# Kernel optimization log

Measured on AMD Instinct MI355X. Metric: run time of the kernel, lower is better.

## Reference

```python
import jax, jax.numpy as jnp
import numpy as np

B, LQ, S, D, H = 8, 1024, 256, 1024, 16
HD = D // H
LN_EPS = 1e-5


def layer_norm(x, g, b):
    m = jnp.mean(x, axis=-1, keepdims=True)
    v = jnp.mean((x - m) ** 2, axis=-1, keepdims=True)
    return (x - m) / jnp.sqrt(v + LN_EPS) * g + b


def setup_inputs() -> dict:
    key = jax.random.key(0)
    ks = jax.random.split(key, 12)
    sc = 0.02
    p = lambda k, shp: jax.random.normal(k, shp, dtype=jnp.float32) * sc
    return {
        "memory": jax.random.normal(ks[0], (B, LQ, D // 2), dtype=jnp.float32),
        "gaze_features": jax.random.normal(ks[1], (B, LQ, D // 2), dtype=jnp.float32),
        "text_features": jax.random.normal(ks[2], (B, S, D), dtype=jnp.float32),
        "w_in": p(ks[3], (3 * D, D)),  # packed q,k,v in_proj (torch MHA layout)
        "b_in": jnp.zeros((3 * D,), jnp.float32),
        "w_o": p(ks[4], (D, D)),
        "b_o": jnp.zeros((D,), jnp.float32),
        "w1": p(ks[5], (D, D)),
        "b1": jnp.zeros((D,), jnp.float32),
        "w2": p(ks[6], (D, D)),
        "b2": jnp.zeros((D,), jnp.float32),
        "g1": jnp.ones((D,), jnp.float32),
        "be1": jnp.zeros((D,), jnp.float32),
        "g2": jnp.ones((D,), jnp.float32),
        "be2": jnp.zeros((D,), jnp.float32),
    }


def reference(memory, gaze_features, text_features, w_in, b_in, w_o, b_o,
              w1, b1, w2, b2, g1, be1, g2, be2):
    combined = jnp.concatenate([memory, gaze_features], axis=-1)  # [B, LQ, D]
    wq, wk, wv = w_in[:D], w_in[D:2 * D], w_in[2 * D:]
    bq, bk, bv = b_in[:D], b_in[D:2 * D], b_in[2 * D:]

    q = (combined @ wq.T + bq).reshape(B, LQ, H, HD)
    k = (text_features @ wk.T + bk).reshape(B, S, H, HD)
    v = (text_features @ wv.T + bv).reshape(B, S, H, HD)

    scores = jnp.einsum("bqhd,bkhd->bhqk", q, k) / jnp.sqrt(jnp.float32(HD))
    attn_w = jax.nn.softmax(scores, axis=-1)
    ctx = jnp.einsum("bhqk,bkhd->bqhd", attn_w, v).reshape(B, LQ, D)
    attn_output = ctx @ w_o.T + b_o  # [B, LQ, D]

    # dual FFN branches share linear1/linear2 (as in the source); dropout = eval identity
    ffn = jax.nn.relu(attn_output @ w1.T + b1) @ w2.T + b2
    refpoint_embed = layer_norm(ffn, g1, be1)
    tgt = layer_norm(ffn, g2, be2)

    # vectorized box decode (replaces the per-element Python loop)
    s = jax.nn.sigmoid(attn_output[..., :4])
    xc, yc, w, h = s[..., 0], s[..., 1], s[..., 2], s[..., 3]
    init_box_proposal = jnp.stack(
        [xc - w / 2, yc - h / 2, xc + w / 2, yc + h / 2], axis=-1)  # [B, LQ, 4]

    return refpoint_embed, tgt, init_box_proposal
```

## Files before the change

kernel.cpp:

```cpp
#include <hip/hip_runtime.h>


typedef unsigned short u16;
typedef unsigned int u32;
typedef __bf16 bf16x8 __attribute__((ext_vector_type(8)));
typedef float f32x4 __attribute__((ext_vector_type(4)));
typedef u16 u16x4 __attribute__((ext_vector_type(4)));

struct CvtArgs { const void* in[15]; };

__device__ __forceinline__ u16 f2bf(float f) {
  u32 u = __builtin_bit_cast(u32, f);
  u += 0x7fffu + ((u >> 16) & 1u);
  return (u16)(u >> 16);
}
__device__ __forceinline__ float bf2f(u16 h) {
  u32 u = ((u32)h) << 16;
  return __builtin_bit_cast(float, u);
}

struct WsPtrs {
  u16 *c_mem, *c_gaze, *c_text, *c_win, *c_bin, *c_wo, *c_bo, *c_w1, *c_b1,
      *c_w2, *c_b2, *c_g1, *c_be1, *c_g2, *c_be2;
  u16 *q, *k, *v, *ctx, *woT, *wf, *bfb, *h1, *ffnb;
};
__device__ __forceinline__ WsPtrs wsp(u16* C) {
  WsPtrs w;
  w.c_mem = C;                 w.c_gaze = C + 4194304;   w.c_text = C + 8388608;
  w.c_win = C + 10485760;      w.c_bin = C + 13631488;   w.c_wo = C + 13634560;
  w.c_bo = C + 14683136;       w.c_w1 = C + 14684160;    w.c_b1 = C + 15732736;
  w.c_w2 = C + 15733760;       w.c_b2 = C + 16782336;    w.c_g1 = C + 16783360;
  w.c_be1 = C + 16784384;      w.c_g2 = C + 16785408;    w.c_be2 = C + 16786432;
  u16* B2 = C + 16787488;
  w.q = B2;                    w.k = B2 + 8388608;       w.v = B2 + 10485760;
  w.ctx = B2 + 12582912;
  w.woT = B2 + 20971520;
  w.wf  = B2 + 22020096;
  w.bfb = B2 + 23068672;
  w.h1  = B2 + 29360128;
  w.ffnb = B2;
  return w;
}

__device__ __forceinline__ void cvt_chunk(bool f32in, u16* dst,
                                          const void* const* srcs, u32 c8) {
  const u32 cum[16] = {0u, 4194304u, 8388608u, 10485760u, 13631488u, 13634560u,
                       14683136u, 14684160u, 15732736u, 15733760u, 16782336u,
                       16783360u, 16784384u, 16785408u, 16786432u, 16787456u};
  u32 base = c8 * 8u;
  int idx = 0;
#pragma unroll
  for (int i = 1; i < 15; ++i) if (base >= cum[i]) idx = i;
  u32 off = base - cum[idx];
  if (f32in) {
    const float* s = (const float*)srcs[idx] + off;
    float4 a = ((const float4*)s)[0];
    float4 b = ((const float4*)s)[1];
    u16 t[8] = {f2bf(a.x), f2bf(a.y), f2bf(a.z), f2bf(a.w),
                f2bf(b.x), f2bf(b.y), f2bf(b.z), f2bf(b.w)};
    *(uint4*)(dst + base) = *(const uint4*)t;
  } else {
    *(uint4*)(dst + base) = *(const uint4*)((const u16*)srcs[idx] + off);
  }
}

__global__ __launch_bounds__(256) void cvt_tr(CvtArgs a, u16* ws) {
  __shared__ u16 tile[128 * 136];
  const bool f32in = (((const u32*)a.in[11])[0] == 0x3F800000u);
  const int bid = blockIdx.x, tid = threadIdx.x;
  if (bid < 64) {
    WsPtrs w = wsp(ws);
    int tr = bid >> 3, tc = bid & 7;
#pragma unroll
    for (int p = 0; p < 8; ++p) {
      int t = p * 16 + (tid >> 4);
      int j8 = (tid & 15) * 8;
      u16 tmp[8];
      if (f32in) {
        const float* s = (const float*)a.in[5] + (size_t)(tr * 128 + t) * 1024 + tc * 128 + j8;
        float4 x = ((const float4*)s)[0], y = ((const float4*)s)[1];
        tmp[0]=f2bf(x.x); tmp[1]=f2bf(x.y); tmp[2]=f2bf(x.z); tmp[3]=f2bf(x.w);
        tmp[4]=f2bf(y.x); tmp[5]=f2bf(y.y); tmp[6]=f2bf(y.z); tmp[7]=f2bf(y.w);
      } else {
        *(uint4*)tmp = *(const uint4*)((const u16*)a.in[5] + (size_t)(tr * 128 + t) * 1024 + tc * 128 + j8);
      }
      *(uint4*)&tile[t * 136 + j8] = *(const uint4*)tmp;
    }
    __syncthreads();
#pragma unroll
    for (int p = 0; p < 8; ++p) {
      int j = p * 16 + (tid >> 4);
      int t8 = (tid & 15) * 8;
      u16 tmp[8];
#pragma unroll
      for (int i = 0; i < 8; ++i) tmp[i] = tile[(t8 + i) * 136 + j];
      *(uint4*)(w.woT + (size_t)(tc * 128 + j) * 1024 + tr * 128 + t8) = *(const uint4*)tmp;
    }
  } else {
    u32 c8 = (u32)(bid - 64) * 256u + tid;
    if (c8 < 2098432u) cvt_chunk(f32in, ws, a.in, c8);
  }
}

__device__ __forceinline__ void gemm_core(
    u16* sA, u16* sB,
    const u16* A0, const u16* A1, int Ksplit, int lda0, int lda1,
    const u16* W, const u16* bias, void* out, int N, int K,
    int mode, int lg, int m0, int n0)
{
  const int tid = threadIdx.x;
  const int wave = tid >> 6, lane = tid & 63;
  const int quad = lane >> 4, l16 = lane & 15;
  const int wm = wave >> 1, wn = wave & 1;

  f32x4 acc[4][4];
#pragma unroll
  for (int i = 0; i < 4; ++i)
#pragma unroll
    for (int j = 0; j < 4; ++j) acc[i][j] = (f32x4){0.f, 0.f, 0.f, 0.f};

  for (int k0 = 0; k0 < K; k0 += 64) {
#pragma unroll
    for (int qi = 0; qi < 4; ++qi) {
      int p = (wave * 4 + qi) * 64 + lane;
      int row = p >> 3;
      int c = (p & 7) ^ (row & 7);
      int gk = k0 + (c << 3);
      const u16* srcA = (gk < Ksplit) ? (A0 + (size_t)(m0 + row) * lda0 + gk)
                                      : (A1 + (size_t)(m0 + row) * lda1 + (gk - Ksplit));
      __builtin_amdgcn_global_load_lds(
          (const __attribute__((address_space(1))) void*)srcA,
          (__attribute__((address_space(3))) void*)&sA[(size_t)(wave * 4 + qi) * 512],
          16, 0, 0);
      const u16* srcB = W + (size_t)(n0 + row) * K + gk;
      __builtin_amdgcn_global_load_lds(
          (const __attribute__((address_space(1))) void*)srcB,
          (__attribute__((address_space(3))) void*)&sB[(size_t)(wave * 4 + qi) * 512],
          16, 0, 0);
    }
    __syncthreads();
#pragma unroll
    for (int ks = 0; ks < 2; ++ks) {
      const int ch = (ks << 2) + quad;
      bf16x8 af[4], bw[4];
#pragma unroll
      for (int i = 0; i < 4; ++i) {
        int row = wm * 64 + i * 16 + l16;
        af[i] = *(const bf16x8*)&sA[(row << 6) + ((ch ^ (row & 7)) << 3)];
      }
#pragma unroll
      for (int j = 0; j < 4; ++j) {
        int row = wn * 64 + j * 16 + l16;
        bw[j] = *(const bf16x8*)&sB[(row << 6) + ((ch ^ (row & 7)) << 3)];
      }
#pragma unroll
      for (int i = 0; i < 4; ++i)
#pragma unroll
        for (int j = 0; j < 4; ++j)
          acc[i][j] = __builtin_amdgcn_mfma_f32_16x16x32_bf16(af[i], bw[j], acc[i][j], 0, 0, 0);
    }
    __syncthreads();
  }

#pragma unroll
  for (int i = 0; i < 4; ++i) {
#pragma unroll
    for (int j = 0; j < 4; ++j) {
      int n = n0 + wn * 64 + j * 16 + l16;
      float bv = bias ? bf2f(bias[n]) : 0.f;
#pragma unroll
      for (int rr = 0; rr < 4; ++rr) {
        int m = m0 + wm * 64 + i * 16 + quad * 4 + rr;
        float val = acc[i][j][rr] + bv;
        if (mode == 1) val = fmaxf(val, 0.f);
        if (mode <= 1) {
          ((u16*)out)[(size_t)m * N + n] = f2bf(val);
        } else if (mode == 3) {
          int b = m >> lg, l = m & ((1 << lg) - 1);
          int h = n >> 6, d = n & 63;
          ((u16*)out)[((size_t)((b * 16 + h)) << (lg + 6)) + (l << 6) + d] = f2bf(val);
        } else {
          int b = m >> lg, s = m & ((1 << lg) - 1);
          int h = n >> 6, d = n & 63;
          ((u16*)out)[((size_t)(((b * 16 + h) << 6) + d) << lg) + s] = f2bf(val);
        }
      }
    }
  }
}

__global__ __launch_bounds__(256, 4) void qkvwf(u16* ws) {
  __shared__ __align__(16) u16 lds[16384];
  WsPtrs w = wsp(ws);
  const int bid = blockIdx.x, tid = threadIdx.x;
  if (bid < 512) {
    gemm_core(lds, lds + 8192, w.c_mem, w.c_gaze, 512, 512, 512,
              w.c_win, w.c_bin, w.q, 1024, 1024, 3, 10,
              (bid >> 3) * 128, (bid & 7) * 128);
  } else if (bid < 640) {
    int u = bid - 512;
    gemm_core(lds, lds + 8192, w.c_text, w.c_text, 1024, 1024, 1024,
              w.c_win + 1048576, w.c_bin + 1024, w.k, 1024, 1024, 3, 8,
              (u >> 3) * 128, (u & 7) * 128);
  } else if (bid < 768) {
    int u = bid - 640;
    gemm_core(lds, lds + 8192, w.c_text, w.c_text, 1024, 1024, 1024,
              w.c_win + 2097152, w.c_bin + 2048, w.v, 1024, 1024, 4, 8,
              (u >> 3) * 128, (u & 7) * 128);
  } else if (bid < 832) {
    int u = bid - 768;
    gemm_core(lds, lds + 8192, w.c_w1, w.c_w1, 1024, 1024, 1024,
              w.woT, nullptr, w.wf, 1024, 1024, 0, 0,
              (u >> 3) * 128, (u & 7) * 128);
  } else {
    int i = (bid - 832) * 256 + tid;
    const u16* w1row = w.c_w1 + (size_t)i * 1024;
    float acc = bf2f(w.c_b1[i]);
    for (int kk = 0; kk < 1024; kk += 8) {
      bf16x8 wv = *(const bf16x8*)(w1row + kk);
      bf16x8 bv = *(const bf16x8*)(w.c_bo + kk);
#pragma unroll
      for (int j = 0; j < 8; ++j) acc += (float)wv[j] * (float)bv[j];
    }
    w.bfb[i] = f2bf(acc);
  }
}

__global__ __launch_bounds__(256) void attn_kernel(u16* ws) {
  __shared__ u16 sV[64 * 256];
  __shared__ u16 sKP[256 * 64];
  WsPtrs w = wsp(ws);
  const int tid = threadIdx.x;
  const int wave = tid >> 6, lane = tid & 63;
  const int quad = lane >> 4, l16 = lane & 15;
  const int qb = blockIdx.x & 15, bh = blockIdx.x >> 4;

  {
    int rr = tid >> 3, c8 = (tid & 7) << 3;
    const u16* kb = w.k + (size_t)bh * 16384;
#pragma unroll
    for (int p = 0; p < 8; ++p) {
      int row = p * 32 + rr;
      uint4 val = *(const uint4*)(kb + row * 64 + c8);
      *(uint4*)&sKP[(row << 6) + ((((c8 >> 3) ^ (row & 7))) << 3)] = val;
    }
    int r2 = tid >> 5, c8b = (tid & 31) << 3;
    const u16* vb = w.v + (size_t)bh * 16384;
#pragma unroll
    for (int p = 0; p < 8; ++p) {
      int row = p * 8 + r2;
      uint4 val = *(const uint4*)(vb + (row << 8) + c8b);
      *(uint4*)&sV[(row << 8) + ((((c8b >> 3) ^ (row & 7))) << 3)] = val;
    }
  }
  bf16x8 aq[2];
  {
    const u16* qrow = w.q + ((size_t)bh * 1024 + qb * 64 + wave * 16 + l16) * 64 + quad * 8;
    aq[0] = *(const bf16x8*)(qrow);
    aq[1] = *(const bf16x8*)(qrow + 32);
  }
  __syncthreads();

  f32x4 sc[16];
#pragma unroll
  for (int nt = 0; nt < 16; ++nt) sc[nt] = (f32x4){0.f, 0.f, 0.f, 0.f};
#pragma unroll
  for (int ks = 0; ks < 2; ++ks) {
    const int ch = (ks << 2) + quad;
#pragma unroll
    for (int nt = 0; nt < 16; ++nt) {
      int row = nt * 16 + l16;
      bf16x8 bk = *(const bf16x8*)&sKP[(row << 6) + ((ch ^ (row & 7)) << 3)];
      sc[nt] = __builtin_amdgcn_mfma_f32_16x16x32_bf16(aq[ks], bk, sc[nt], 0, 0, 0);
    }
  }
#pragma unroll
  for (int rr = 0; rr < 4; ++rr) {
    float mx = -1e30f;
#pragma unroll
    for (int nt = 0; nt < 16; ++nt) mx = fmaxf(mx, sc[nt][rr]);
    for (int off = 1; off < 16; off <<= 1) mx = fmaxf(mx, __shfl_xor(mx, off, 64));
    float sum = 0.f;
#pragma unroll
    for (int nt = 0; nt < 16; ++nt) {
      float p = __expf((sc[nt][rr] - mx) * 0.125f);
      sc[nt][rr] = p; sum += p;
    }
    for (int off = 1; off < 16; off <<= 1) sum += __shfl_xor(sum, off, 64);
    float inv = 1.f / sum;
#pragma unroll
    for (int nt = 0; nt < 16; ++nt) sc[nt][rr] *= inv;
  }
  __syncthreads();
#pragma unroll
  for (int nt = 0; nt < 16; ++nt)
#pragma unroll
    for (int rr = 0; rr < 4; ++rr) {
      int row = wave * 16 + quad * 4 + rr;
      int col = nt * 16 + l16;
      sKP[(row << 8) + (((col >> 3) ^ (row & 7)) << 3) + (col & 7)] = f2bf(sc[nt][rr]);
    }
  __syncthreads();

  f32x4 o[4];
#pragma unroll
  for (int j = 0; j < 4; ++j) o[j] = (f32x4){0.f, 0.f, 0.f, 0.f};
#pragma unroll
  for (int ks = 0; ks < 8; ++ks) {
    const int ch = (ks << 2) + quad;
    int prow = wave * 16 + l16;
    bf16x8 ap = *(const bf16x8*)&sKP[(prow << 8) + ((ch ^ (prow & 7)) << 3)];
#pragma unroll
    for (int j = 0; j < 4; ++j) {
      int vrow = j * 16 + l16;
      bf16x8 bv = *(const bf16x8*)&sV[(vrow << 8) + ((ch ^ (vrow & 7)) << 3)];
      o[j] = __builtin_amdgcn_mfma_f32_16x16x32_bf16(ap, bv, o[j], 0, 0, 0);
    }
  }
  const int b = bh >> 4, h = bh & 15;
#pragma unroll
  for (int j = 0; j < 4; ++j)
#pragma unroll
    for (int rr = 0; rr < 4; ++rr) {
      int m = qb * 64 + wave * 16 + quad * 4 + rr;
      int d = h * 64 + j * 16 + l16;
      w.ctx[((size_t)b * 1024 + m) * 1024 + d] = f2bf(o[j][rr]);
    }
}

__global__ __launch_bounds__(256, 4) void h1box(u16* ws, void* out, const void* g1orig) {
  __shared__ __align__(16) u16 lds[16384];
  WsPtrs w = wsp(ws);
  const int u = blockIdx.x, tid = threadIdx.x;
  const int r16 = tid >> 4, l4 = tid & 15;
  {
    const bool f32out = (((const u32*)g1orig)[0] == 0x3F800000u);
    int m = u * 16 + r16;
    int k0 = l4 * 64;
    const u16* crow = w.ctx + (size_t)m * 1024 + k0;
    float a0 = 0.f, a1 = 0.f, a2 = 0.f, a3 = 0.f;
#pragma unroll
    for (int kk = 0; kk < 64; kk += 8) {
      bf16x8 cv = *(const bf16x8*)(crow + kk);
      bf16x8 w0 = *(const bf16x8*)(w.c_wo + k0 + kk);
      bf16x8 w1 = *(const bf16x8*)(w.c_wo + 1024 + k0 + kk);
      bf16x8 w2 = *(const bf16x8*)(w.c_wo + 2048 + k0 + kk);
      bf16x8 w3 = *(const bf16x8*)(w.c_wo + 3072 + k0 + kk);
#pragma unroll
      for (int j = 0; j < 8; ++j) {
        float c = (float)cv[j];
        a0 += c * (float)w0[j]; a1 += c * (float)w1[j];
        a2 += c * (float)w2[j]; a3 += c * (float)w3[j];
      }
    }
    for (int off = 1; off < 16; off <<= 1) {
      a0 += __shfl_xor(a0, off, 64); a1 += __shfl_xor(a1, off, 64);
      a2 += __shfl_xor(a2, off, 64); a3 += __shfl_xor(a3, off, 64);
    }
    if (l4 == 0) {
      a0 += bf2f(w.c_bo[0]); a1 += bf2f(w.c_bo[1]);
      a2 += bf2f(w.c_bo[2]); a3 += bf2f(w.c_bo[3]);
      float s0 = 1.f / (1.f + __expf(-a0)), s1 = 1.f / (1.f + __expf(-a1));
      float s2 = 1.f / (1.f + __expf(-a2)), s3 = 1.f / (1.f + __expf(-a3));
      float o0 = s0 - s2 * 0.5f, o1 = s1 - s3 * 0.5f;
      float o2 = s0 + s2 * 0.5f, o3 = s1 + s3 * 0.5f;
      if (f32out) {
        float* fo = (float*)out + 16777216;
        *(float4*)(fo + (size_t)m * 4) = make_float4(o0, o1, o2, o3);
      } else {
        u16* bo = (u16*)out + 16777216;
        u16x4 o; o[0] = f2bf(o0); o[1] = f2bf(o1); o[2] = f2bf(o2); o[3] = f2bf(o3);
        *(u16x4*)(bo + (size_t)m * 4) = o;
      }
    }
  }
  gemm_core(lds, lds + 8192, w.ctx, w.ctx, 1024, 1024, 1024,
            w.wf, w.bfb, w.h1, 1024, 1024, 1, 0, (u >> 3) * 128, (u & 7) * 128);
}

__global__ __launch_bounds__(256, 4) void w2gemm(u16* ws) {
  __shared__ __align__(16) u16 lds[16384];
  WsPtrs w = wsp(ws);
  gemm_core(lds, lds + 8192, w.h1, w.h1, 1024, 1024, 1024,
            w.c_w2, w.c_b2, w.ffnb, 1024, 1024, 0, 0,
            (blockIdx.x >> 3) * 128, (blockIdx.x & 7) * 128);
}

__global__ __launch_bounds__(256) void ln_kernel(u16* ws, void* outv, const void* g1orig) {
  WsPtrs w = wsp(ws);
  const bool f32out = (((const u32*)g1orig)[0] == 0x3F800000u);
  const int row = blockIdx.x, tid = threadIdx.x;
  int c = tid * 4;
  u16x4 xr = *(const u16x4*)(w.ffnb + (size_t)row * 1024 + c);
  float x[4] = {bf2f(xr[0]), bf2f(xr[1]), bf2f(xr[2]), bf2f(xr[3])};
  float s = x[0] + x[1] + x[2] + x[3];
  float s2 = x[0]*x[0] + x[1]*x[1] + x[2]*x[2] + x[3]*x[3];
  for (int m = 32; m >= 1; m >>= 1) { s += __shfl_xor(s, m, 64); s2 += __shfl_xor(s2, m, 64); }
  __shared__ float red[8];
  int wv = tid >> 6;
  if ((tid & 63) == 0) { red[wv] = s; red[4 + wv] = s2; }
  __syncthreads();
  s = red[0] + red[1] + red[2] + red[3];
  s2 = red[4] + red[5] + red[6] + red[7];
  float mean = s * (1.f / 1024.f);
  float var = s2 * (1.f / 1024.f) - mean * mean;
  float inv = rsqrtf(var + 1e-5f);
  float y[4] = {(x[0] - mean) * inv, (x[1] - mean) * inv, (x[2] - mean) * inv, (x[3] - mean) * inv};
  float v1[4], v2[4];
#pragma unroll
  for (int i = 0; i < 4; ++i) {
    v1[i] = y[i] * bf2f(w.c_g1[c + i]) + bf2f(w.c_be1[c + i]);
    v2[i] = y[i] * bf2f(w.c_g2[c + i]) + bf2f(w.c_be2[c + i]);
  }
  if (f32out) {
    float* fo = (float*)outv;
    *(float4*)(fo + (size_t)row * 1024 + c) = make_float4(v1[0], v1[1], v1[2], v1[3]);
    *(float4*)(fo + 8388608 + (size_t)row * 1024 + c) = make_float4(v2[0], v2[1], v2[2], v2[3]);
  } else {
    u16* out = (u16*)outv;
    u16x4 o1, o2;
#pragma unroll
    for (int i = 0; i < 4; ++i) { o1[i] = f2bf(v1[i]); o2[i] = f2bf(v2[i]); }
    *(u16x4*)(out + (size_t)row * 1024 + c) = o1;
    *(u16x4*)(out + 8388608 + (size_t)row * 1024 + c) = o2;
  }
}

extern "C" void kernel_launch(void* const* d_in, const int* in_sizes, int n_in,
                              void* d_out, int out_size, void* d_ws, size_t ws_size,
                              hipStream_t stream) {
  CvtArgs ca;
  for (int i = 0; i < 15; ++i) ca.in[i] = d_in[i];
  u16* ws = (u16*)d_ws;
  dim3 blk(256);
  cvt_tr<<<dim3(8261), blk, 0, stream>>>(ca, ws);
  qkvwf<<<dim3(836), blk, 0, stream>>>(ws);
  attn_kernel<<<dim3(2048), blk, 0, stream>>>(ws);
  h1box<<<dim3(512), blk, 0, stream>>>(ws, d_out, d_in[11]);
  w2gemm<<<dim3(512), blk, 0, stream>>>(ws);
  ln_kernel<<<dim3(8192), blk, 0, stream>>>(ws, d_out, d_in[11]);
}
```

Before: 300.3 us.

## Template GEMM K-tile, use BK=128 for FFN GEMMs, add block swizzle and setprio

Makes the GEMM core generic over the K tile depth and switches the two FFN GEMMs to a 128-wide K tile with doubled LDS, which halves the number of barrier-separated K iterations. Block indices in every GEMM and in attention are remapped with an XCD-style swizzle so that neighbouring tiles land on the same chiplet and share L2. Attention MFMA sections are wrapped in s_setprio. The larger LDS footprint and the removed occupancy hint can lower occupancy in the FFN GEMMs.

```diff
diff --git a/kernel.cpp b/kernel.cpp
--- a/kernel.cpp
+++ b/kernel.cpp
@@ -102,12 +102,16 @@
   }
 }
 
+template <int BK>
 __device__ __forceinline__ void gemm_core(
     u16* sA, u16* sB,
     const u16* A0, const u16* A1, int Ksplit, int lda0, int lda1,
     const u16* W, const u16* bias, void* out, int N, int K,
     int mode, int lg, int m0, int n0)
 {
+  constexpr int CPT = BK / 16;
+  constexpr int LGC = (BK == 64) ? 3 : 4;
+  constexpr int LGR = (BK == 64) ? 6 : 7;
   const int tid = threadIdx.x;
   const int wave = tid >> 6, lane = tid & 63;
   const int quad = lane >> 4, l16 = lane & 15;
@@ -119,39 +123,39 @@
 #pragma unroll
     for (int j = 0; j < 4; ++j) acc[i][j] = (f32x4){0.f, 0.f, 0.f, 0.f};
 
-  for (int k0 = 0; k0 < K; k0 += 64) {
-#pragma unroll
-    for (int qi = 0; qi < 4; ++qi) {
-      int p = (wave * 4 + qi) * 64 + lane;
-      int row = p >> 3;
-      int c = (p & 7) ^ (row & 7);
+  for (int k0 = 0; k0 < K; k0 += BK) {
+#pragma unroll
+    for (int qi = 0; qi < CPT; ++qi) {
+      int p = (wave * CPT + qi) * 64 + lane;
+      int row = p >> LGC;
+      int c = (p & ((1 << LGC) - 1)) ^ (row & 7);
       int gk = k0 + (c << 3);
       const u16* srcA = (gk < Ksplit) ? (A0 + (size_t)(m0 + row) * lda0 + gk)
                                       : (A1 + (size_t)(m0 + row) * lda1 + (gk - Ksplit));
       __builtin_amdgcn_global_load_lds(
           (const __attribute__((address_space(1))) void*)srcA,
-          (__attribute__((address_space(3))) void*)&sA[(size_t)(wave * 4 + qi) * 512],
+          (__attribute__((address_space(3))) void*)&sA[(size_t)(wave * CPT + qi) * 512],
           16, 0, 0);
       const u16* srcB = W + (size_t)(n0 + row) * K + gk;
       __builtin_amdgcn_global_load_lds(
           (const __attribute__((address_space(1))) void*)srcB,
-          (__attribute__((address_space(3))) void*)&sB[(size_t)(wave * 4 + qi) * 512],
+          (__attribute__((address_space(3))) void*)&sB[(size_t)(wave * CPT + qi) * 512],
           16, 0, 0);
     }
     __syncthreads();
 #pragma unroll
-    for (int ks = 0; ks < 2; ++ks) {
+    for (int ks = 0; ks < BK / 32; ++ks) {
       const int ch = (ks << 2) + quad;
       bf16x8 af[4], bw[4];
 #pragma unroll
       for (int i = 0; i < 4; ++i) {
         int row = wm * 64 + i * 16 + l16;
-        af[i] = *(const bf16x8*)&sA[(row << 6) + ((ch ^ (row & 7)) << 3)];
+        af[i] = *(const bf16x8*)&sA[(row << LGR) + ((ch ^ (row & 7)) << 3)];
       }
 #pragma unroll
       for (int j = 0; j < 4; ++j) {
         int row = wn * 64 + j * 16 + l16;
-        bw[j] = *(const bf16x8*)&sB[(row << 6) + ((ch ^ (row & 7)) << 3)];
+        bw[j] = *(const bf16x8*)&sB[(row << LGR) + ((ch ^ (row & 7)) << 3)];
       }
 #pragma unroll
       for (int i = 0; i < 4; ++i)
@@ -189,29 +193,34 @@
   }
 }
 
+__device__ __forceinline__ int xswz(int u, int n8) {
+  return (u & 7) * n8 + (u >> 3);
+}
+
 __global__ __launch_bounds__(256, 4) void qkvwf(u16* ws) {
   __shared__ __align__(16) u16 lds[16384];
   WsPtrs w = wsp(ws);
   const int bid = blockIdx.x, tid = threadIdx.x;
   if (bid < 512) {
-    gemm_core(lds, lds + 8192, w.c_mem, w.c_gaze, 512, 512, 512,
-              w.c_win, w.c_bin, w.q, 1024, 1024, 3, 10,
-              (bid >> 3) * 128, (bid & 7) * 128);
+    int u = xswz(bid, 64);
+    gemm_core<64>(lds, lds + 8192, w.c_mem, w.c_gaze, 512, 512, 512,
+                  w.c_win, w.c_bin, w.q, 1024, 1024, 3, 10,
+                  (u >> 3) * 128, (u & 7) * 128);
   } else if (bid < 640) {
-    int u = bid - 512;
-    gemm_core(lds, lds + 8192, w.c_text, w.c_text, 1024, 1024, 1024,
-              w.c_win + 1048576, w.c_bin + 1024, w.k, 1024, 1024, 3, 8,
-              (u >> 3) * 128, (u & 7) * 128);
+    int u = xswz(bid - 512, 16);
+    gemm_core<64>(lds, lds + 8192, w.c_text, w.c_text, 1024, 1024, 1024,
+                  w.c_win + 1048576, w.c_bin + 1024, w.k, 1024, 1024, 3, 8,
+                  (u >> 3) * 128, (u & 7) * 128);
   } else if (bid < 768) {
-    int u = bid - 640;
-    gemm_core(lds, lds + 8192, w.c_text, w.c_text, 1024, 1024, 1024,
-              w.c_win + 2097152, w.c_bin + 2048, w.v, 1024, 1024, 4, 8,
-              (u >> 3) * 128, (u & 7) * 128);
+    int u = xswz(bid - 640, 16);
+    gemm_core<64>(lds, lds + 8192, w.c_text, w.c_text, 1024, 1024, 1024,
+                  w.c_win + 2097152, w.c_bin + 2048, w.v, 1024, 1024, 4, 8,
+                  (u >> 3) * 128, (u & 7) * 128);
   } else if (bid < 832) {
-    int u = bid - 768;
-    gemm_core(lds, lds + 8192, w.c_w1, w.c_w1, 1024, 1024, 1024,
-              w.woT, nullptr, w.wf, 1024, 1024, 0, 0,
-              (u >> 3) * 128, (u & 7) * 128);
+    int u = xswz(bid - 768, 8);
+    gemm_core<64>(lds, lds + 8192, w.c_w1, w.c_w1, 1024, 1024, 1024,
+                  w.woT, nullptr, w.wf, 1024, 1024, 0, 0,
+                  (u >> 3) * 128, (u & 7) * 128);
   } else {
     int i = (bid - 832) * 256 + tid;
     const u16* w1row = w.c_w1 + (size_t)i * 1024;
@@ -233,7 +242,8 @@
   const int tid = threadIdx.x;
   const int wave = tid >> 6, lane = tid & 63;
   const int quad = lane >> 4, l16 = lane & 15;
-  const int qb = blockIdx.x & 15, bh = blockIdx.x >> 4;
+  const int su = xswz(blockIdx.x, 256);
+  const int qb = su & 15, bh = su >> 4;
 
   {
     int rr = tid >> 3, c8 = (tid & 7) << 3;
@@ -264,6 +274,7 @@
   f32x4 sc[16];
 #pragma unroll
   for (int nt = 0; nt < 16; ++nt) sc[nt] = (f32x4){0.f, 0.f, 0.f, 0.f};
+  __builtin_amdgcn_s_setprio(1);
 #pragma unroll
   for (int ks = 0; ks < 2; ++ks) {
     const int ch = (ks << 2) + quad;
@@ -274,6 +285,7 @@
       sc[nt] = __builtin_amdgcn_mfma_f32_16x16x32_bf16(aq[ks], bk, sc[nt], 0, 0, 0);
     }
   }
+  __builtin_amdgcn_s_setprio(0);
 #pragma unroll
   for (int rr = 0; rr < 4; ++rr) {
     float mx = -1e30f;
@@ -305,6 +317,7 @@
   f32x4 o[4];
 #pragma unroll
   for (int j = 0; j < 4; ++j) o[j] = (f32x4){0.f, 0.f, 0.f, 0.f};
+  __builtin_amdgcn_s_setprio(1);
 #pragma unroll
   for (int ks = 0; ks < 8; ++ks) {
     const int ch = (ks << 2) + quad;
@@ -317,6 +330,7 @@
       o[j] = __builtin_amdgcn_mfma_f32_16x16x32_bf16(ap, bv, o[j], 0, 0, 0);
     }
   }
+  __builtin_amdgcn_s_setprio(0);
   const int b = bh >> 4, h = bh & 15;
 #pragma unroll
   for (int j = 0; j < 4; ++j)
@@ -328,8 +342,8 @@
     }
 }
 
-__global__ __launch_bounds__(256, 4) void h1box(u16* ws, void* out, const void* g1orig) {
-  __shared__ __align__(16) u16 lds[16384];
+__global__ __launch_bounds__(256) void h1box(u16* ws, void* out, const void* g1orig) {
+  __shared__ __align__(16) u16 lds[32768];
   WsPtrs w = wsp(ws);
   const int u = blockIdx.x, tid = threadIdx.x;
   const int r16 = tid >> 4, l4 = tid & 15;
@@ -374,16 +388,19 @@
       }
     }
   }
-  gemm_core(lds, lds + 8192, w.ctx, w.ctx, 1024, 1024, 1024,
-            w.wf, w.bfb, w.h1, 1024, 1024, 1, 0, (u >> 3) * 128, (u & 7) * 128);
-}
-
-__global__ __launch_bounds__(256, 4) void w2gemm(u16* ws) {
-  __shared__ __align__(16) u16 lds[16384];
+  int us = xswz(u, 64);
+  gemm_core<128>(lds, lds + 16384, w.ctx, w.ctx, 1024, 1024, 1024,
+                 w.wf, w.bfb, w.h1, 1024, 1024, 1, 0,
+                 (us >> 3) * 128, (us & 7) * 128);
+}
+
+__global__ __launch_bounds__(256) void w2gemm(u16* ws) {
+  __shared__ __align__(16) u16 lds[32768];
   WsPtrs w = wsp(ws);
-  gemm_core(lds, lds + 8192, w.h1, w.h1, 1024, 1024, 1024,
-            w.c_w2, w.c_b2, w.ffnb, 1024, 1024, 0, 0,
-            (blockIdx.x >> 3) * 128, (blockIdx.x & 7) * 128);
+  int us = xswz((int)blockIdx.x, 64);
+  gemm_core<128>(lds, lds + 16384, w.h1, w.h1, 1024, 1024, 1024,
+                 w.c_w2, w.c_b2, w.ffnb, 1024, 1024, 0, 0,
+                 (us >> 3) * 128, (us & 7) * 128);
 }
 
 __global__ __launch_bounds__(256) void ln_kernel(u16* ws, void* outv, const void* g1orig) {
```

New measurement: 289.4 us. 1.04x faster.
